# Kernel tuning notes

Measured on AMD Instinct MI355X. Metric: run time of the kernel, lower is better.

The kernel has to match this reference:

```python
import jax, jax.numpy as jnp
import numpy as np

EMBED = 384
N_HEADS = 6
HEAD_SIZE = EMBED // N_HEADS
B, T = 4, 2048
EPS = 1e-5


def _layernorm(x, g, b):
    mu = jnp.mean(x, axis=-1, keepdims=True)
    var = jnp.mean(jnp.square(x - mu), axis=-1, keepdims=True)
    return (x - mu) * jax.lax.rsqrt(var + EPS) * g + b


def setup_inputs() -> dict:
    key = jax.random.key(0)
    ks = jax.random.split(key, 6)
    s = 0.02
    return {
        "x": jax.random.normal(ks[0], (B, T, EMBED), jnp.float32),
        "Wq": jax.random.normal(ks[1], (N_HEADS, HEAD_SIZE, EMBED), jnp.float32) * s,
        "Wo": jax.random.normal(ks[2], (EMBED, EMBED), jnp.float32) * s,
        "bo": jnp.zeros((EMBED,), jnp.float32),
        "W1": jax.random.normal(ks[3], (EMBED, EMBED), jnp.float32) * s,
        "b1": jnp.zeros((EMBED,), jnp.float32),
        "W2": jax.random.normal(ks[4], (EMBED, EMBED), jnp.float32) * s,
        "b2": jnp.zeros((EMBED,), jnp.float32),
        "g1": jnp.ones((EMBED,), jnp.float32),
        "be1": jnp.zeros((EMBED,), jnp.float32),
        "g2": jnp.ones((EMBED,), jnp.float32),
        "be2": jnp.zeros((EMBED,), jnp.float32),
    }


def reference(x, Wq, Wo, bo, W1, b1, W2, b2, g1, be1, g2, be2):
    # NOTE: original Head uses self.query for q, k AND v (a bug we reproduce):
    # q = k = v = x @ Wq^T per head.
    q = jnp.einsum("bte,hde->bhtd", x, Wq)  # [B,H,T,D]
    scale = HEAD_SIZE ** -0.5
    scores = jnp.einsum("bhtd,bhsd->bhts", q, q) * scale  # [B,H,T,T]
    # torch.tril zeros the upper triangle, then masked_fill(tmp==0, -inf)
    tril = jnp.tril(jnp.ones((T, T), bool))
    scores = jnp.where(tril, scores, 0.0)
    scores = jnp.where(scores == 0.0, -jnp.inf, scores)
    attn = jax.nn.softmax(scores, axis=-1)
    head_out = jnp.einsum("bhts,bhsd->bhtd", attn, q)  # [B,H,T,D]
    cat = head_out.transpose(0, 2, 1, 3).reshape(B, T, EMBED)  # concat heads
    sa = cat @ Wo.T + bo
    x = _layernorm(x + sa, g1, be1)
    ff = jax.nn.relu(x @ W1.T + b1) @ W2.T + b2
    return _layernorm(x + ff, g2, be2)
```

## Files before the change

kernel.cpp:

```cpp
#include <hip/hip_runtime.h>
#include <math.h>

#define BB 4
#define TT 2048
#define EE 384
#define HH 6
#define DD 64
#define MM (BB*TT)

typedef __attribute__((ext_vector_type(8))) short bf16x8;
typedef __attribute__((ext_vector_type(4))) float f32x4;

__device__ __forceinline__ unsigned short f2bf(float f) {
    unsigned int u = __float_as_uint(f);
    u = (u + 0x7FFFu + ((u >> 16) & 1u)) >> 16;
    return (unsigned short)u;
}
__device__ __forceinline__ float bf2f(unsigned short u) {
    return __uint_as_float(((unsigned int)u) << 16);
}
__device__ __forceinline__ unsigned int pk2(float a, float b) {
    return (unsigned int)f2bf(a) | ((unsigned int)f2bf(b) << 16);
}

__global__ __launch_bounds__(256) void k_cvt(const float* __restrict__ wq,
                                             const float* __restrict__ wo,
                                             const float* __restrict__ w1,
                                             const float* __restrict__ w2,
                                             unsigned short* __restrict__ wqb,
                                             unsigned short* __restrict__ wob,
                                             unsigned short* __restrict__ w1b,
                                             unsigned short* __restrict__ w2b)
{
    int wi = blockIdx.x / 144, off = (blockIdx.x % 144) * 256;
    const float* s4[4] = {wq, wo, w1, w2};
    unsigned short* d4[4] = {wqb, wob, w1b, w2b};
    const float* src = s4[wi]; unsigned short* dst = d4[wi];
    int i = off + threadIdx.x;
    float4 v = ((const float4*)src)[i];
    uint2 o; o.x = pk2(v.x, v.y); o.y = pk2(v.z, v.w);
    ((uint2*)dst)[i] = o;
}

__global__ __launch_bounds__(256, 4) void k_qgemm(const float* __restrict__ A,
                                                  const unsigned short* __restrict__ W,
                                                  unsigned short* __restrict__ qbf)
{
    const int tid = threadIdx.x;
    const int w = tid >> 6, lane = tid & 63;
    const int fr = lane & 15, quad = lane >> 4;
    const int m0 = blockIdx.x * 16;
    const int n0 = blockIdx.y * 192 + w * 48;
    const float* Ap = A + (size_t)(m0 + fr) * EE + quad * 8;
    const unsigned short* Wp = W + (size_t)(n0 + fr) * EE + quad * 8;

    f32x4 acc[3];
    #pragma unroll
    for (int nt = 0; nt < 3; nt++) acc[nt] = (f32x4){0.f, 0.f, 0.f, 0.f};

    #pragma unroll
    for (int k0 = 0; k0 < 12; k0++) {
        float4 a0 = *(const float4*)(Ap + k0 * 32);
        float4 a1 = *(const float4*)(Ap + k0 * 32 + 4);
        unsigned int ap[4];
        ap[0] = pk2(a0.x, a0.y); ap[1] = pk2(a0.z, a0.w);
        ap[2] = pk2(a1.x, a1.y); ap[3] = pk2(a1.z, a1.w);
        bf16x8 a = *(const bf16x8*)ap;
        #pragma unroll
        for (int nt = 0; nt < 3; nt++) {
            bf16x8 b = *(const bf16x8*)(Wp + (size_t)nt * 16 * EE + k0 * 32);
            acc[nt] = __builtin_amdgcn_mfma_f32_16x16x32_bf16(a, b, acc[nt], 0, 0, 0);
        }
    }

    const int mrow = m0 + quad * 4;
    #pragma unroll
    for (int nt = 0; nt < 3; nt++) {
        int n = n0 + nt * 16 + fr;
        int h = n >> 6, d = n & 63;
        #pragma unroll
        for (int r = 0; r < 4; r++) {
            int m = mrow + r;
            int b = m >> 11, t = m & 2047;
            qbf[((size_t)(b * HH + h) * TT + t) * DD + d] = f2bf(acc[nt][r]);
        }
    }
}

__global__ __launch_bounds__(256) void k_prep(const unsigned short* __restrict__ qbf,
                                              unsigned short* __restrict__ qbfT)
{
    __shared__ unsigned short Ls[64][72];
    const int bh = blockIdx.y;
    const int t0 = blockIdx.x * 64;
    const unsigned short* src = qbf + ((size_t)bh * TT + t0) * DD;
    {
        int r = threadIdx.x >> 2, c = (threadIdx.x & 3) * 16;
        const unsigned short* p = src + (size_t)r * DD + c;
        *(uint4*)&Ls[r][c]     = *(const uint4*)(p);
        *(uint4*)&Ls[r][c + 8] = *(const uint4*)(p + 8);
    }
    __syncthreads();
    {
        int d = threadIdx.x >> 2, tc = (threadIdx.x & 3) * 16;
        unsigned short tmp[16];
        #pragma unroll
        for (int i = 0; i < 16; i++) tmp[i] = Ls[tc + i][d];
        unsigned short* dst = qbfT + ((size_t)bh * DD + d) * TT + t0 + tc;
        *(uint4*)(dst)     = *(const uint4*)&tmp[0];
        *(uint4*)(dst + 8) = *(const uint4*)&tmp[8];
    }
}

__global__ __launch_bounds__(256, 4) void k_attn(const unsigned short* __restrict__ qbf,
                                                 const unsigned short* __restrict__ qbfT,
                                                 unsigned short* __restrict__ cat)
{
    __shared__ unsigned short Qs[32][72];
    __shared__ unsigned short Ks[64][72];
    __shared__ unsigned short Vs[64][72];
    __shared__ unsigned short Ps[32][72];
    __shared__ float Oc[32][68];
    __shared__ float lsc[32];
    const int p = blockIdx.x;
    const int bh = blockIdx.y;
    const int bb = bh / HH, hh = bh % HH;
    const int tid = threadIdx.x;
    const int w = tid >> 6, lane = tid & 63;
    const int qhalf = w & 1, keyhalf = w >> 1;
    const int fr = lane & 15, quad = lane >> 4;
    const int fc = quad * 8;
    const unsigned short* qb  = qbf  + (size_t)bh * TT * DD;
    const unsigned short* qtb = qbfT + (size_t)bh * DD * TT;
    const int lr = tid >> 2, lc = (tid & 3) * 16;
    const int qr = tid >> 3, qc = (tid & 7) * 8;

    #pragma unroll 1
    for (int ph = 0; ph < 2; ph++) {
        const int tile = ph ? (63 - p) : p;
        const int m0 = tile * 32;
        const int nkt = (tile >> 1) + 1;

        uint4 kr0, kr1, vr0, vr1;
        {
            const unsigned short* kp = qb + (size_t)lr * DD + lc;
            kr0 = *(const uint4*)(kp);
            kr1 = *(const uint4*)(kp + 8);
            const unsigned short* vp = qtb + (size_t)lr * TT + lc;
            vr0 = *(const uint4*)(vp);
            vr1 = *(const uint4*)(vp + 8);
        }

        __syncthreads();
        {
            const unsigned short* qp = qb + (size_t)(m0 + qr) * DD + qc;
            *(uint4*)&Qs[qr][qc] = *(const uint4*)(qp);
        }
        __syncthreads();
        const bf16x8 qA0 = *(const bf16x8*)&Qs[qhalf * 16 + fr][fc];
        const bf16x8 qA1 = *(const bf16x8*)&Qs[qhalf * 16 + fr][fc + 32];

        f32x4 accO[4];
        #pragma unroll
        for (int dt = 0; dt < 4; dt++) accO[dt] = (f32x4){0.f, 0.f, 0.f, 0.f};
        float ls[4] = {0.f, 0.f, 0.f, 0.f};
        const int rowbase = m0 + qhalf * 16 + quad * 4;
        const int prow = qhalf * 16 + quad * 4;

        for (int kt = 0; kt < nkt; kt++) {
            const int s0 = kt * 64;
            __syncthreads();
            *(uint4*)&Ks[lr][lc]     = kr0;
            *(uint4*)&Ks[lr][lc + 8] = kr1;
            *(uint4*)&Vs[lr][lc]     = vr0;
            *(uint4*)&Vs[lr][lc + 8] = vr1;
            if (kt < nkt - 1) {
                const unsigned short* kp = qb + (size_t)(s0 + 64 + lr) * DD + lc;
                kr0 = *(const uint4*)(kp);
                kr1 = *(const uint4*)(kp + 8);
                const unsigned short* vp = qtb + (size_t)lr * TT + s0 + 64 + lc;
                vr0 = *(const uint4*)(vp);
                vr1 = *(const uint4*)(vp + 8);
            }
            __syncthreads();

            f32x4 S[2];
            #pragma unroll
            for (int nt = 0; nt < 2; nt++) {
                f32x4 acc = (f32x4){0.f, 0.f, 0.f, 0.f};
                bf16x8 b0 = *(const bf16x8*)&Ks[keyhalf * 32 + nt * 16 + fr][fc];
                acc = __builtin_amdgcn_mfma_f32_16x16x32_bf16(qA0, b0, acc, 0, 0, 0);
                bf16x8 b1 = *(const bf16x8*)&Ks[keyhalf * 32 + nt * 16 + fr][fc + 32];
                acc = __builtin_amdgcn_mfma_f32_16x16x32_bf16(qA1, b1, acc, 0, 0, 0);
                S[nt] = acc;
            }

            #pragma unroll
            for (int nt = 0; nt < 2; nt++) {
                int jg = s0 + keyhalf * 32 + nt * 16 + fr;
                #pragma unroll
                for (int r = 0; r < 4; r++) {
                    float v = S[nt][r] * 0.125f;
                    float pv = (jg <= rowbase + r && v != 0.0f) ? __expf(v) : 0.0f;
                    ls[r] += pv;
                    Ps[prow + r][keyhalf * 32 + nt * 16 + fr] = f2bf(pv);
                }
            }

            bf16x8 pA = *(const bf16x8*)&Ps[qhalf * 16 + fr][keyhalf * 32 + fc];
            #pragma unroll
            for (int dt = 0; dt < 4; dt++) {
                bf16x8 v0 = *(const bf16x8*)&Vs[dt * 16 + fr][keyhalf * 32 + fc];
                accO[dt] = __builtin_amdgcn_mfma_f32_16x16x32_bf16(pA, v0, accO[dt], 0, 0, 0);
            }
        }

        #pragma unroll
        for (int r = 0; r < 4; r++) {
            #pragma unroll
            for (int o = 1; o < 16; o <<= 1) ls[r] += __shfl_xor(ls[r], o, 64);
        }
        if (keyhalf == 1) {
            #pragma unroll
            for (int dt = 0; dt < 4; dt++)
                #pragma unroll
                for (int r = 0; r < 4; r++)
                    Oc[prow + r][dt * 16 + fr] = accO[dt][r];
            if (fr == 0) {
                #pragma unroll
                for (int r = 0; r < 4; r++) lsc[prow + r] = ls[r];
            }
        }
        __syncthreads();
        if (keyhalf == 0) {
            float lt[4];
            #pragma unroll
            for (int r = 0; r < 4; r++) lt[r] = ls[r] + lsc[prow + r];
            #pragma unroll
            for (int dt = 0; dt < 4; dt++) {
                #pragma unroll
                for (int r = 0; r < 4; r++) {
                    float o = accO[dt][r] + Oc[prow + r][dt * 16 + fr];
                    int t = rowbase + r;
                    cat[((size_t)bb * TT + t) * EE + hh * DD + dt * 16 + fr] =
                        f2bf(o / lt[r]);
                }
            }
        }
    }
}

__global__ __launch_bounds__(256, 2) void k_ffn(const unsigned short* __restrict__ catb,
                                                const unsigned short* __restrict__ wob,
                                                const float* __restrict__ bo,
                                                const float* __restrict__ x,
                                                const float* __restrict__ g1,
                                                const float* __restrict__ be1,
                                                const unsigned short* __restrict__ w1b,
                                                const float* __restrict__ b1,
                                                const unsigned short* __restrict__ w2b,
                                                const float* __restrict__ b2,
                                                const float* __restrict__ g2,
                                                const float* __restrict__ be2,
                                                float* __restrict__ out)
{
    __shared__ unsigned short X1s[32][392];
    __shared__ unsigned short H1s[32][392];
    __shared__ float ssum[32][4];
    __shared__ float ssq[32][4];
    const int tid = threadIdx.x;
    const int w = tid >> 6, lane = tid & 63;
    const int fr = lane & 15, quad = lane >> 4;
    const int m0 = blockIdx.x * 32;
    const int n0 = w * 96;

    f32x4 acc[2][6];
    bf16x8 bc[6], bn[6];

    {
        const unsigned short* Ap0 = catb + (size_t)(m0 + fr) * EE + quad * 8;
        const unsigned short* Ap1 = Ap0 + 16 * EE;
        const unsigned short* Wp = wob + (size_t)(n0 + fr) * EE + quad * 8;
        #pragma unroll
        for (int mt = 0; mt < 2; mt++)
            #pragma unroll
            for (int nt = 0; nt < 6; nt++) acc[mt][nt] = (f32x4){0.f, 0.f, 0.f, 0.f};
        #pragma unroll
        for (int nt = 0; nt < 6; nt++) bc[nt] = *(const bf16x8*)(Wp + (size_t)nt * 16 * EE);
        #pragma unroll
        for (int k0 = 0; k0 < 12; k0++) {
            if (k0 < 11) {
                #pragma unroll
                for (int nt = 0; nt < 6; nt++)
                    bn[nt] = *(const bf16x8*)(Wp + (size_t)nt * 16 * EE + (k0 + 1) * 32);
            }
            bf16x8 a0 = *(const bf16x8*)(Ap0 + k0 * 32);
            bf16x8 a1 = *(const bf16x8*)(Ap1 + k0 * 32);
            #pragma unroll
            for (int nt = 0; nt < 6; nt++) {
                acc[0][nt] = __builtin_amdgcn_mfma_f32_16x16x32_bf16(a0, bc[nt], acc[0][nt], 0, 0, 0);
                acc[1][nt] = __builtin_amdgcn_mfma_f32_16x16x32_bf16(a1, bc[nt], acc[1][nt], 0, 0, 0);
            }
            #pragma unroll
            for (int nt = 0; nt < 6; nt++) bc[nt] = bn[nt];
        }
    }
    {
        float s1[2][4] = {{0.f,0.f,0.f,0.f},{0.f,0.f,0.f,0.f}};
        float s2[2][4] = {{0.f,0.f,0.f,0.f},{0.f,0.f,0.f,0.f}};
        #pragma unroll
        for (int nt = 0; nt < 6; nt++) {
            int n = n0 + nt * 16 + fr;
            float bv = bo[n];
            #pragma unroll
            for (int mt = 0; mt < 2; mt++)
                #pragma unroll
                for (int r = 0; r < 4; r++) {
                    float v = acc[mt][nt][r] + bv
                            + x[(size_t)(m0 + mt * 16 + quad * 4 + r) * EE + n];
                    acc[mt][nt][r] = v;
                    s1[mt][r] += v;
                    s2[mt][r] += v * v;
                }
        }
        #pragma unroll
        for (int mt = 0; mt < 2; mt++)
            #pragma unroll
            for (int r = 0; r < 4; r++) {
                #pragma unroll
                for (int o = 1; o < 16; o <<= 1) {
                    s1[mt][r] += __shfl_xor(s1[mt][r], o, 64);
                    s2[mt][r] += __shfl_xor(s2[mt][r], o, 64);
                }
            }
        if (fr == 0) {
            #pragma unroll
            for (int mt = 0; mt < 2; mt++)
                #pragma unroll
                for (int r = 0; r < 4; r++) {
                    ssum[mt * 16 + quad * 4 + r][w] = s1[mt][r];
                    ssq [mt * 16 + quad * 4 + r][w] = s2[mt][r];
                }
        }
    }
    __syncthreads();
    {
        #pragma unroll
        for (int mt = 0; mt < 2; mt++) {
            float mu[4], rs[4];
            #pragma unroll
            for (int r = 0; r < 4; r++) {
                int row = mt * 16 + quad * 4 + r;
                float t1 = ssum[row][0] + ssum[row][1] + ssum[row][2] + ssum[row][3];
                float t2 = ssq[row][0] + ssq[row][1] + ssq[row][2] + ssq[row][3];
                mu[r] = t1 * (1.0f / EE);
                float var = t2 * (1.0f / EE) - mu[r] * mu[r];
                rs[r] = rsqrtf(var + 1e-5f);
            }
            #pragma unroll
            for (int nt = 0; nt < 6; nt++) {
                int n = n0 + nt * 16 + fr;
                float gv = g1[n], bev = be1[n];
                #pragma unroll
                for (int r = 0; r < 4; r++) {
                    float v = (acc[mt][nt][r] - mu[r]) * rs[r] * gv + bev;
                    X1s[mt * 16 + quad * 4 + r][n] = f2bf(v);
                }
            }
        }
    }
    __syncthreads();

    {
        const unsigned short* Wp = w1b + (size_t)(n0 + fr) * EE + quad * 8;
        #pragma unroll
        for (int mt = 0; mt < 2; mt++)
            #pragma unroll
            for (int nt = 0; nt < 6; nt++) acc[mt][nt] = (f32x4){0.f, 0.f, 0.f, 0.f};
        #pragma unroll
        for (int nt = 0; nt < 6; nt++) bc[nt] = *(const bf16x8*)(Wp + (size_t)nt * 16 * EE);
        #pragma unroll
        for (int k0 = 0; k0 < 12; k0++) {
            if (k0 < 11) {
                #pragma unroll
                for (int nt = 0; nt < 6; nt++)
                    bn[nt] = *(const bf16x8*)(Wp + (size_t)nt * 16 * EE + (k0 + 1) * 32);
            }
            bf16x8 a0 = *(const bf16x8*)&X1s[fr][k0 * 32 + quad * 8];
            bf16x8 a1 = *(const bf16x8*)&X1s[16 + fr][k0 * 32 + quad * 8];
            #pragma unroll
            for (int nt = 0; nt < 6; nt++) {
                acc[0][nt] = __builtin_amdgcn_mfma_f32_16x16x32_bf16(a0, bc[nt], acc[0][nt], 0, 0, 0);
                acc[1][nt] = __builtin_amdgcn_mfma_f32_16x16x32_bf16(a1, bc[nt], acc[1][nt], 0, 0, 0);
            }
            #pragma unroll
            for (int nt = 0; nt < 6; nt++) bc[nt] = bn[nt];
        }
        #pragma unroll
        for (int nt = 0; nt < 6; nt++) {
            int n = n0 + nt * 16 + fr;
            float bv = b1[n];
            #pragma unroll
            for (int mt = 0; mt < 2; mt++)
                #pragma unroll
                for (int r = 0; r < 4; r++)
                    H1s[mt * 16 + quad * 4 + r][n] = f2bf(fmaxf(acc[mt][nt][r] + bv, 0.0f));
        }
    }
    __syncthreads();

    {
        const unsigned short* Wp = w2b + (size_t)(n0 + fr) * EE + quad * 8;
        #pragma unroll
        for (int mt = 0; mt < 2; mt++)
            #pragma unroll
            for (int nt = 0; nt < 6; nt++) acc[mt][nt] = (f32x4){0.f, 0.f, 0.f, 0.f};
        #pragma unroll
        for (int nt = 0; nt < 6; nt++) bc[nt] = *(const bf16x8*)(Wp + (size_t)nt * 16 * EE);
        #pragma unroll
        for (int k0 = 0; k0 < 12; k0++) {
            if (k0 < 11) {
                #pragma unroll
                for (int nt = 0; nt < 6; nt++)
                    bn[nt] = *(const bf16x8*)(Wp + (size_t)nt * 16 * EE + (k0 + 1) * 32);
            }
            bf16x8 a0 = *(const bf16x8*)&H1s[fr][k0 * 32 + quad * 8];
            bf16x8 a1 = *(const bf16x8*)&H1s[16 + fr][k0 * 32 + quad * 8];
            #pragma unroll
            for (int nt = 0; nt < 6; nt++) {
                acc[0][nt] = __builtin_amdgcn_mfma_f32_16x16x32_bf16(a0, bc[nt], acc[0][nt], 0, 0, 0);
                acc[1][nt] = __builtin_amdgcn_mfma_f32_16x16x32_bf16(a1, bc[nt], acc[1][nt], 0, 0, 0);
            }
            #pragma unroll
            for (int nt = 0; nt < 6; nt++) bc[nt] = bn[nt];
        }
    }
    {
        float s1[2][4] = {{0.f,0.f,0.f,0.f},{0.f,0.f,0.f,0.f}};
        float s2[2][4] = {{0.f,0.f,0.f,0.f},{0.f,0.f,0.f,0.f}};
        #pragma unroll
        for (int nt = 0; nt < 6; nt++) {
            int n = n0 + nt * 16 + fr;
            float bv = b2[n];
            #pragma unroll
            for (int mt = 0; mt < 2; mt++)
                #pragma unroll
                for (int r = 0; r < 4; r++) {
                    float v = acc[mt][nt][r] + bv
                            + bf2f(X1s[mt * 16 + quad * 4 + r][n]);
                    acc[mt][nt][r] = v;
                    s1[mt][r] += v;
                    s2[mt][r] += v * v;
                }
        }
        #pragma unroll
        for (int mt = 0; mt < 2; mt++)
            #pragma unroll
            for (int r = 0; r < 4; r++) {
                #pragma unroll
                for (int o = 1; o < 16; o <<= 1) {
                    s1[mt][r] += __shfl_xor(s1[mt][r], o, 64);
                    s2[mt][r] += __shfl_xor(s2[mt][r], o, 64);
                }
            }
        if (fr == 0) {
            #pragma unroll
            for (int mt = 0; mt < 2; mt++)
                #pragma unroll
                for (int r = 0; r < 4; r++) {
                    ssum[mt * 16 + quad * 4 + r][w] = s1[mt][r];
                    ssq [mt * 16 + quad * 4 + r][w] = s2[mt][r];
                }
        }
    }
    __syncthreads();
    {
        #pragma unroll
        for (int mt = 0; mt < 2; mt++) {
            float mu[4], rs[4];
            #pragma unroll
            for (int r = 0; r < 4; r++) {
                int row = mt * 16 + quad * 4 + r;
                float u1 = ssum[row][0] + ssum[row][1] + ssum[row][2] + ssum[row][3];
                float u2 = ssq[row][0] + ssq[row][1] + ssq[row][2] + ssq[row][3];
                mu[r] = u1 * (1.0f / EE);
                float var = u2 * (1.0f / EE) - mu[r] * mu[r];
                rs[r] = rsqrtf(var + 1e-5f);
            }
            #pragma unroll
            for (int nt = 0; nt < 6; nt++) {
                int n = n0 + nt * 16 + fr;
                float gv = g2[n], bev = be2[n];
                #pragma unroll
                for (int r = 0; r < 4; r++)
                    out[(size_t)(m0 + mt * 16 + quad * 4 + r) * EE + n] =
                        (acc[mt][nt][r] - mu[r]) * rs[r] * gv + bev;
            }
        }
    }
}

extern "C" void kernel_launch(void* const* d_in, const int* in_sizes, int n_in,
                              void* d_out, int out_size, void* d_ws, size_t ws_size,
                              hipStream_t stream) {
    (void)in_sizes; (void)n_in; (void)out_size; (void)ws_size;
    const float* x   = (const float*)d_in[0];
    const float* Wq  = (const float*)d_in[1];
    const float* Wo  = (const float*)d_in[2];
    const float* bo  = (const float*)d_in[3];
    const float* W1  = (const float*)d_in[4];
    const float* b1  = (const float*)d_in[5];
    const float* W2  = (const float*)d_in[6];
    const float* b2  = (const float*)d_in[7];
    const float* g1  = (const float*)d_in[8];
    const float* be1 = (const float*)d_in[9];
    const float* g2  = (const float*)d_in[10];
    const float* be2 = (const float*)d_in[11];
    float* out = (float*)d_out;

    float* ws = (float*)d_ws;
    const size_t SZ = (size_t)MM * EE;
    float* S1 = ws + SZ;
    float* S2 = ws + 2 * SZ;
    float* S3 = ws + 3 * SZ;

    unsigned short* qbf  = (unsigned short*)S1;
    unsigned short* qbfT = qbf + (size_t)BB * HH * TT * DD;
    unsigned short* catb = (unsigned short*)S2;
    unsigned short* wqb  = (unsigned short*)S3;
    unsigned short* wob  = wqb + (size_t)EE * EE;
    unsigned short* w1b  = wob + (size_t)EE * EE;
    unsigned short* w2b  = w1b + (size_t)EE * EE;

    k_cvt<<<dim3(4 * 144), dim3(256), 0, stream>>>(Wq, Wo, W1, W2, wqb, wob, w1b, w2b);
    k_qgemm<<<dim3(MM / 16, 2), dim3(256), 0, stream>>>(x, wqb, qbf);
    k_prep<<<dim3(TT / 64, BB * HH), dim3(256), 0, stream>>>(qbf, qbfT);
    k_attn<<<dim3(32, BB * HH), dim3(256), 0, stream>>>(qbf, qbfT, catb);
    k_ffn<<<dim3(MM / 32), dim3(256), 0, stream>>>(catb, wob, bo, x, g1, be1,
                                                   w1b, b1, w2b, b2, g2, be2, out);
}
```

Measured before the change: 204.7 us.

## Transpose V in attention LDS and widen FFN blocks to 8 waves

Removes the separate k_prep transpose kernel and its global qbfT buffer. The attention kernel now builds the transposed V tile in shared memory from the K registers it already loads, using a rotated scatter to spread LDS bank conflicts. This saves one launch and a full read and write of Q in global memory, at the cost of 16 scalar LDS stores per thread per key tile. Separately, k_ffn runs 512 threads, each wave covering 48 columns instead of 96, which halves accumulator and register pressure per wave and widens the LayerNorm partial-sum arrays to 8.

```diff
diff --git a/kernel.cpp b/kernel.cpp
--- a/kernel.cpp
+++ b/kernel.cpp
@@ -87,33 +87,7 @@
     }
 }
 
-__global__ __launch_bounds__(256) void k_prep(const unsigned short* __restrict__ qbf,
-                                              unsigned short* __restrict__ qbfT)
-{
-    __shared__ unsigned short Ls[64][72];
-    const int bh = blockIdx.y;
-    const int t0 = blockIdx.x * 64;
-    const unsigned short* src = qbf + ((size_t)bh * TT + t0) * DD;
-    {
-        int r = threadIdx.x >> 2, c = (threadIdx.x & 3) * 16;
-        const unsigned short* p = src + (size_t)r * DD + c;
-        *(uint4*)&Ls[r][c]     = *(const uint4*)(p);
-        *(uint4*)&Ls[r][c + 8] = *(const uint4*)(p + 8);
-    }
-    __syncthreads();
-    {
-        int d = threadIdx.x >> 2, tc = (threadIdx.x & 3) * 16;
-        unsigned short tmp[16];
-        #pragma unroll
-        for (int i = 0; i < 16; i++) tmp[i] = Ls[tc + i][d];
-        unsigned short* dst = qbfT + ((size_t)bh * DD + d) * TT + t0 + tc;
-        *(uint4*)(dst)     = *(const uint4*)&tmp[0];
-        *(uint4*)(dst + 8) = *(const uint4*)&tmp[8];
-    }
-}
-
 __global__ __launch_bounds__(256, 4) void k_attn(const unsigned short* __restrict__ qbf,
-                                                 const unsigned short* __restrict__ qbfT,
                                                  unsigned short* __restrict__ cat)
 {
     __shared__ unsigned short Qs[32][72];
@@ -130,9 +104,9 @@
     const int qhalf = w & 1, keyhalf = w >> 1;
     const int fr = lane & 15, quad = lane >> 4;
     const int fc = quad * 8;
-    const unsigned short* qb  = qbf  + (size_t)bh * TT * DD;
-    const unsigned short* qtb = qbfT + (size_t)bh * DD * TT;
+    const unsigned short* qb = qbf + (size_t)bh * TT * DD;
     const int lr = tid >> 2, lc = (tid & 3) * 16;
+    const int rot = (tid & 3) * 2;
     const int qr = tid >> 3, qc = (tid & 7) * 8;
 
     #pragma unroll 1
@@ -141,14 +115,11 @@
         const int m0 = tile * 32;
         const int nkt = (tile >> 1) + 1;
 
-        uint4 kr0, kr1, vr0, vr1;
+        uint4 kr0, kr1;
         {
             const unsigned short* kp = qb + (size_t)lr * DD + lc;
             kr0 = *(const uint4*)(kp);
             kr1 = *(const uint4*)(kp + 8);
-            const unsigned short* vp = qtb + (size_t)lr * TT + lc;
-            vr0 = *(const uint4*)(vp);
-            vr1 = *(const uint4*)(vp + 8);
         }
 
         __syncthreads();
@@ -172,15 +143,20 @@
             __syncthreads();
             *(uint4*)&Ks[lr][lc]     = kr0;
             *(uint4*)&Ks[lr][lc + 8] = kr1;
-            *(uint4*)&Vs[lr][lc]     = vr0;
-            *(uint4*)&Vs[lr][lc + 8] = vr1;
+            {
+                unsigned short tmp[16];
+                *(uint4*)&tmp[0] = kr0;
+                *(uint4*)&tmp[8] = kr1;
+                #pragma unroll
+                for (int i = 0; i < 16; i++) {
+                    int j = (i + rot) & 15;
+                    Vs[lc + j][lr] = tmp[j];
+                }
+            }
             if (kt < nkt - 1) {
                 const unsigned short* kp = qb + (size_t)(s0 + 64 + lr) * DD + lc;
                 kr0 = *(const uint4*)(kp);
                 kr1 = *(const uint4*)(kp + 8);
-                const unsigned short* vp = qtb + (size_t)lr * TT + s0 + 64 + lc;
-                vr0 = *(const uint4*)(vp);
-                vr1 = *(const uint4*)(vp + 8);
             }
             __syncthreads();
 
@@ -250,7 +226,7 @@
     }
 }
 
-__global__ __launch_bounds__(256, 2) void k_ffn(const unsigned short* __restrict__ catb,
+__global__ __launch_bounds__(512, 2) void k_ffn(const unsigned short* __restrict__ catb,
                                                 const unsigned short* __restrict__ wob,
                                                 const float* __restrict__ bo,
                                                 const float* __restrict__ x,
@@ -266,16 +242,16 @@
 {
     __shared__ unsigned short X1s[32][392];
     __shared__ unsigned short H1s[32][392];
-    __shared__ float ssum[32][4];
-    __shared__ float ssq[32][4];
+    __shared__ float ssum[32][8];
+    __shared__ float ssq[32][8];
     const int tid = threadIdx.x;
     const int w = tid >> 6, lane = tid & 63;
     const int fr = lane & 15, quad = lane >> 4;
     const int m0 = blockIdx.x * 32;
-    const int n0 = w * 96;
-
-    f32x4 acc[2][6];
-    bf16x8 bc[6], bn[6];
+    const int n0 = w * 48;
+
+    f32x4 acc[2][3];
+    bf16x8 bc[3], bn[3];
 
     {
         const unsigned short* Ap0 = catb + (size_t)(m0 + fr) * EE + quad * 8;
@@ -284,32 +260,32 @@
         #pragma unroll
         for (int mt = 0; mt < 2; mt++)
             #pragma unroll
-            for (int nt = 0; nt < 6; nt++) acc[mt][nt] = (f32x4){0.f, 0.f, 0.f, 0.f};
-        #pragma unroll
-        for (int nt = 0; nt < 6; nt++) bc[nt] = *(const bf16x8*)(Wp + (size_t)nt * 16 * EE);
+            for (int nt = 0; nt < 3; nt++) acc[mt][nt] = (f32x4){0.f, 0.f, 0.f, 0.f};
+        #pragma unroll
+        for (int nt = 0; nt < 3; nt++) bc[nt] = *(const bf16x8*)(Wp + (size_t)nt * 16 * EE);
         #pragma unroll
         for (int k0 = 0; k0 < 12; k0++) {
             if (k0 < 11) {
                 #pragma unroll
-                for (int nt = 0; nt < 6; nt++)
+                for (int nt = 0; nt < 3; nt++)
                     bn[nt] = *(const bf16x8*)(Wp + (size_t)nt * 16 * EE + (k0 + 1) * 32);
             }
             bf16x8 a0 = *(const bf16x8*)(Ap0 + k0 * 32);
             bf16x8 a1 = *(const bf16x8*)(Ap1 + k0 * 32);
             #pragma unroll
-            for (int nt = 0; nt < 6; nt++) {
+            for (int nt = 0; nt < 3; nt++) {
                 acc[0][nt] = __builtin_amdgcn_mfma_f32_16x16x32_bf16(a0, bc[nt], acc[0][nt], 0, 0, 0);
                 acc[1][nt] = __builtin_amdgcn_mfma_f32_16x16x32_bf16(a1, bc[nt], acc[1][nt], 0, 0, 0);
             }
             #pragma unroll
-            for (int nt = 0; nt < 6; nt++) bc[nt] = bn[nt];
+            for (int nt = 0; nt < 3; nt++) bc[nt] = bn[nt];
         }
     }
     {
         float s1[2][4] = {{0.f,0.f,0.f,0.f},{0.f,0.f,0.f,0.f}};
         float s2[2][4] = {{0.f,0.f,0.f,0.f},{0.f,0.f,0.f,0.f}};
         #pragma unroll
-        for (int nt = 0; nt < 6; nt++) {
+        for (int nt = 0; nt < 3; nt++) {
             int n = n0 + nt * 16 + fr;
             float bv = bo[n];
             #pragma unroll
@@ -351,14 +327,15 @@
             #pragma unroll
             for (int r = 0; r < 4; r++) {
                 int row = mt * 16 + quad * 4 + r;
-                float t1 = ssum[row][0] + ssum[row][1] + ssum[row][2] + ssum[row][3];
-                float t2 = ssq[row][0] + ssq[row][1] + ssq[row][2] + ssq[row][3];
+                float t1 = 0.f, t2 = 0.f;
+                #pragma unroll
+                for (int q = 0; q < 8; q++) { t1 += ssum[row][q]; t2 += ssq[row][q]; }
                 mu[r] = t1 * (1.0f / EE);
                 float var = t2 * (1.0f / EE) - mu[r] * mu[r];
                 rs[r] = rsqrtf(var + 1e-5f);
             }
             #pragma unroll
-            for (int nt = 0; nt < 6; nt++) {
+            for (int nt = 0; nt < 3; nt++) {
                 int n = n0 + nt * 16 + fr;
                 float gv = g1[n], bev = be1[n];
                 #pragma unroll
@@ -376,28 +353,28 @@
         #pragma unroll
         for (int mt = 0; mt < 2; mt++)
             #pragma unroll
-            for (int nt = 0; nt < 6; nt++) acc[mt][nt] = (f32x4){0.f, 0.f, 0.f, 0.f};
-        #pragma unroll
-        for (int nt = 0; nt < 6; nt++) bc[nt] = *(const bf16x8*)(Wp + (size_t)nt * 16 * EE);
+            for (int nt = 0; nt < 3; nt++) acc[mt][nt] = (f32x4){0.f, 0.f, 0.f, 0.f};
+        #pragma unroll
+        for (int nt = 0; nt < 3; nt++) bc[nt] = *(const bf16x8*)(Wp + (size_t)nt * 16 * EE);
         #pragma unroll
         for (int k0 = 0; k0 < 12; k0++) {
             if (k0 < 11) {
                 #pragma unroll
-                for (int nt = 0; nt < 6; nt++)
+                for (int nt = 0; nt < 3; nt++)
                     bn[nt] = *(const bf16x8*)(Wp + (size_t)nt * 16 * EE + (k0 + 1) * 32);
             }
             bf16x8 a0 = *(const bf16x8*)&X1s[fr][k0 * 32 + quad * 8];
             bf16x8 a1 = *(const bf16x8*)&X1s[16 + fr][k0 * 32 + quad * 8];
             #pragma unroll
-            for (int nt = 0; nt < 6; nt++) {
+            for (int nt = 0; nt < 3; nt++) {
                 acc[0][nt] = __builtin_amdgcn_mfma_f32_16x16x32_bf16(a0, bc[nt], acc[0][nt], 0, 0, 0);
                 acc[1][nt] = __builtin_amdgcn_mfma_f32_16x16x32_bf16(a1, bc[nt], acc[1][nt], 0, 0, 0);
             }
             #pragma unroll
-            for (int nt = 0; nt < 6; nt++) bc[nt] = bn[nt];
-        }
-        #pragma unroll
-        for (int nt = 0; nt < 6; nt++) {
+            for (int nt = 0; nt < 3; nt++) bc[nt] = bn[nt];
+        }
+        #pragma unroll
+        for (int nt = 0; nt < 3; nt++) {
             int n = n0 + nt * 16 + fr;
             float bv = b1[n];
             #pragma unroll
@@ -414,40 +391,39 @@
         #pragma unroll
         for (int mt = 0; mt < 2; mt++)
             #pragma unroll
-            for (int nt = 0; nt < 6; nt++) acc[mt][nt] = (f32x4){0.f, 0.f, 0.f, 0.f};
-        #pragma unroll
-        for (int nt = 0; nt < 6; nt++) bc[nt] = *(const bf16x8*)(Wp + (size_t)nt * 16 * EE);
+            for (int nt = 0; nt < 3; nt++) acc[mt][nt] = (f32x4){0.f, 0.f, 0.f, 0.f};
+        #pragma unroll
+        for (int nt = 0; nt < 3; nt++) bc[nt] = *(const bf16x8*)(Wp + (size_t)nt * 16 * EE);
         #pragma unroll
         for (int k0 = 0; k0 < 12; k0++) {
             if (k0 < 11) {
                 #pragma unroll
-                for (int nt = 0; nt < 6; nt++)
+                for (int nt = 0; nt < 3; nt++)
                     bn[nt] = *(const bf16x8*)(Wp + (size_t)nt * 16 * EE + (k0 + 1) * 32);
             }
             bf16x8 a0 = *(const bf16x8*)&H1s[fr][k0 * 32 + quad * 8];
             bf16x8 a1 = *(const bf16x8*)&H1s[16 + fr][k0 * 32 + quad * 8];
             #pragma unroll
-            for (int nt = 0; nt < 6; nt++) {
+            for (int nt = 0; nt < 3; nt++) {
                 acc[0][nt] = __builtin_amdgcn_mfma_f32_16x16x32_bf16(a0, bc[nt], acc[0][nt], 0, 0, 0);
                 acc[1][nt] = __builtin_amdgcn_mfma_f32_16x16x32_bf16(a1, bc[nt], acc[1][nt], 0, 0, 0);
             }
             #pragma unroll
-            for (int nt = 0; nt < 6; nt++) bc[nt] = bn[nt];
+            for (int nt = 0; nt < 3; nt++) bc[nt] = bn[nt];
         }
     }
     {
         float s1[2][4] = {{0.f,0.f,0.f,0.f},{0.f,0.f,0.f,0.f}};
         float s2[2][4] = {{0.f,0.f,0.f,0.f},{0.f,0.f,0.f,0.f}};
         #pragma unroll
-        for (int nt = 0; nt < 6; nt++) {
+        for (int nt = 0; nt < 3; nt++) {
             int n = n0 + nt * 16 + fr;
             float bv = b2[n];
             #pragma unroll
             for (int mt = 0; mt < 2; mt++)
                 #pragma unroll
                 for (int r = 0; r < 4; r++) {
-                    float v = acc[mt][nt][r] + bv
-                            + bf2f(X1s[mt * 16 + quad * 4 + r][n]);
+                    float v = acc[mt][nt][r] + bv + bf2f(X1s[mt * 16 + quad * 4 + r][n]);
                     acc[mt][nt][r] = v;
                     s1[mt][r] += v;
                     s2[mt][r] += v * v;
@@ -481,14 +457,15 @@
             #pragma unroll
             for (int r = 0; r < 4; r++) {
                 int row = mt * 16 + quad * 4 + r;
-                float u1 = ssum[row][0] + ssum[row][1] + ssum[row][2] + ssum[row][3];
-                float u2 = ssq[row][0] + ssq[row][1] + ssq[row][2] + ssq[row][3];
+                float u1 = 0.f, u2 = 0.f;
+                #pragma unroll
+                for (int q = 0; q < 8; q++) { u1 += ssum[row][q]; u2 += ssq[row][q]; }
                 mu[r] = u1 * (1.0f / EE);
                 float var = u2 * (1.0f / EE) - mu[r] * mu[r];
                 rs[r] = rsqrtf(var + 1e-5f);
             }
             #pragma unroll
-            for (int nt = 0; nt < 6; nt++) {
+            for (int nt = 0; nt < 3; nt++) {
                 int n = n0 + nt * 16 + fr;
                 float gv = g2[n], bev = be2[n];
                 #pragma unroll
@@ -525,7 +502,6 @@
     float* S3 = ws + 3 * SZ;
 
     unsigned short* qbf  = (unsigned short*)S1;
-    unsigned short* qbfT = qbf + (size_t)BB * HH * TT * DD;
     unsigned short* catb = (unsigned short*)S2;
     unsigned short* wqb  = (unsigned short*)S3;
     unsigned short* wob  = wqb + (size_t)EE * EE;
@@ -534,8 +510,7 @@
 
     k_cvt<<<dim3(4 * 144), dim3(256), 0, stream>>>(Wq, Wo, W1, W2, wqb, wob, w1b, w2b);
     k_qgemm<<<dim3(MM / 16, 2), dim3(256), 0, stream>>>(x, wqb, qbf);
-    k_prep<<<dim3(TT / 64, BB * HH), dim3(256), 0, stream>>>(qbf, qbfT);
-    k_attn<<<dim3(32, BB * HH), dim3(256), 0, stream>>>(qbf, qbfT, catb);
-    k_ffn<<<dim3(MM / 32), dim3(256), 0, stream>>>(catb, wob, bo, x, g1, be1,
+    k_attn<<<dim3(32, BB * HH), dim3(256), 0, stream>>>(qbf, catb);
+    k_ffn<<<dim3(MM / 32), dim3(512), 0, stream>>>(catb, wob, bo, x, g1, be1,
                                                    w1b, b1, w2b, b2, g2, be2, out);
 }
```

After: 266.3 us. 1.3x slower.
